# Kernel tuning notes

Hardware: AMD Instinct MI355X
Metric: run time of the kernel (lower is better)

The kernel has to match this reference:

```python
import jax, jax.numpy as jnp
import numpy as np

D_IN = 1024
D_OUT = 1024
N = 4096


def setup_inputs() -> dict:
    key = jax.random.key(0)
    kx, kq, kk, kv = jax.random.split(key, 4)
    x = jax.random.normal(kx, (N, D_IN), dtype=jnp.float32)
    # weights stored as [d_in, d_out] so that x @ W == torch Linear(x)
    s = 1.0 / np.sqrt(D_IN)
    W_q = jax.random.uniform(kq, (D_IN, D_OUT), jnp.float32, -s, s)
    W_k = jax.random.uniform(kk, (D_IN, D_OUT), jnp.float32, -s, s)
    W_v = jax.random.uniform(kv, (D_IN, D_OUT), jnp.float32, -s, s)
    return {"x": x, "W_q": W_q, "W_k": W_k, "W_v": W_v}


def reference(x, W_q, W_k, W_v):
    # x: [N, d_in]; projections -> [N, d_out]
    q = x @ W_q
    k = x @ W_k
    v = x @ W_v
    scale = 1.0 / jnp.sqrt(jnp.asarray(k.shape[-1], dtype=q.dtype))
    scores = (q @ k.T) * scale            # [N, N]
    weights = jax.nn.softmax(scores, axis=-1)
    return weights @ v                     # [N, d_out]
```

## Files before the change

### kernel.cpp

```cpp
#include <hip/hip_runtime.h>
#include <math.h>

typedef _Float16 f16;
typedef __attribute__((ext_vector_type(8))) _Float16 f16x8;
typedef __attribute__((ext_vector_type(4))) _Float16 f16x4;
typedef __attribute__((ext_vector_type(4))) float f32x4;

#define NSEQ 4096
#define DIN 1024
#define DOUT 1024

__device__ __forceinline__ void load16(const void* g, void* l) {
    __builtin_amdgcn_global_load_lds(
        (const __attribute__((address_space(1))) unsigned int*)g,
        (__attribute__((address_space(3))) unsigned int*)l, 16, 0, 0);
}

template <typename OutT, int EPI>
__global__ __launch_bounds__(256, 2)
void gemm_bt(const f16* __restrict__ A, const f16* __restrict__ B,
             OutT* __restrict__ c0, OutT* __restrict__ c1,
             OutT* __restrict__ c2, OutT* __restrict__ c3,
             int M, int N, int K, int lda, int ldb, int ldc, float scale,
             long aStrideZ, long bStrideZ,
             f16* __restrict__ TC, int tz, int ldt, float* __restrict__ Sums)
{
    const int z = blockIdx.z;
    A += (long)z * aStrideZ;
    B += (long)z * bStrideZ;
    OutT* C = z == 0 ? c0 : (z == 1 ? c1 : (z == 2 ? c2 : c3));
    __shared__ f16 As[2 * 128 * 32];
    __shared__ f16 Bs[2 * 128 * 32];

    int gx = gridDim.x;
    int bid = blockIdx.y * gx + blockIdx.x;
    int xcd = bid & 7, s = bid >> 3;
    int px = s & 7, rest = s >> 3;
    int py = rest & 3, chunk = rest >> 2;
    int pg = xcd + (chunk << 3);
    int pcols = gx >> 3;
    int lp = 31 - __clz(pcols);
    int bx = ((pg & (pcols - 1)) << 3) + px;
    int by = ((pg >> lp) << 2) + py;

    const int t    = threadIdx.x;
    const int lane = t & 63;
    const int wave = t >> 6;
    const int wm   = (wave >> 1) * 64;
    const int wn   = (wave & 1) * 64;
    const int tile_m = by * 128;
    const int tile_n = bx * 128;
    const int quad = lane >> 4;
    const int l16  = lane & 15;
    const int srow = t >> 2;
    const int scol = (((t & 3) + srow + (srow >> 2)) & 3) * 8;
    const int qx8 = ((quad - (l16 + (l16 >> 2))) & 3) * 8;

    f32x4 acc[4][4];
#pragma unroll
    for (int i = 0; i < 4; i++)
#pragma unroll
        for (int j = 0; j < 4; j++)
            acc[i][j] = (f32x4){0.f, 0.f, 0.f, 0.f};

    const f16* Ab = A + (long)(tile_m + srow) * lda + scol;
    const f16* Bb = B + (long)(tile_n + srow) * ldb + scol;
    f16* Asd = As + t * 8;
    f16* Bsd = Bs + t * 8;

    for (int k0 = 0; k0 < K; k0 += 64) {
        load16(Ab + k0, Asd);
        load16(Ab + (long)64 * lda + k0, Asd + 2048);
        load16(Ab + k0 + 32, Asd + 4096);
        load16(Ab + (long)64 * lda + k0 + 32, Asd + 4096 + 2048);
        load16(Bb + k0, Bsd);
        load16(Bb + (long)64 * ldb + k0, Bsd + 2048);
        load16(Bb + k0 + 32, Bsd + 4096);
        load16(Bb + (long)64 * ldb + k0 + 32, Bsd + 4096 + 2048);
        __syncthreads();
#pragma unroll
        for (int p = 0; p < 2; p++) {
            f16x8 a[4], b[4];
#pragma unroll
            for (int i = 0; i < 4; i++)
                a[i] = *(const f16x8*)(As + p * 4096 + (wm + i * 16 + l16) * 32 + qx8);
#pragma unroll
            for (int j = 0; j < 4; j++)
                b[j] = *(const f16x8*)(Bs + p * 4096 + (wn + j * 16 + l16) * 32 + qx8);
#pragma unroll
            for (int i = 0; i < 4; i++)
#pragma unroll
                for (int j = 0; j < 4; j++)
                    acc[i][j] = __builtin_amdgcn_mfma_f32_16x16x32_f16(
                        a[i], b[j], acc[i][j], 0, 0, 0);
        }
        __syncthreads();
    }
    if (EPI == 1) {
        if (z == tz) {
#pragma unroll
            for (int i = 0; i < 4; i++)
#pragma unroll
                for (int j = 0; j < 4; j++) {
                    f16x4 o;
#pragma unroll
                    for (int r = 0; r < 4; r++) o[r] = (f16)(acc[i][j][r] * scale);
                    int row0 = tile_m + wm + i * 16 + quad * 4;
                    int col  = tile_n + wn + j * 16 + l16;
                    *(f16x4*)(TC + (long)col * ldt + row0) = o;
                }
        } else {
#pragma unroll
            for (int i = 0; i < 4; i++)
#pragma unroll
                for (int j = 0; j < 4; j++)
#pragma unroll
                    for (int r = 0; r < 4; r++) {
                        int row = tile_m + wm + i * 16 + quad * 4 + r;
                        int col = tile_n + wn + j * 16 + l16;
                        C[(long)row * ldc + col] = (OutT)(acc[i][j][r] * scale);
                    }
        }
    } else if (EPI == 2) {
        const int bxs = bx * 2 + (wn >> 6);
#pragma unroll
        for (int i = 0; i < 4; i++) {
            float rs[4] = {0.f, 0.f, 0.f, 0.f};
#pragma unroll
            for (int j = 0; j < 4; j++)
#pragma unroll
                for (int r = 0; r < 4; r++) {
                    float e = __expf(acc[i][j][r] * scale);
                    int row = tile_m + wm + i * 16 + quad * 4 + r;
                    int col = tile_n + wn + j * 16 + l16;
                    C[(long)row * ldc + col] = (OutT)e;
                    rs[r] += e;
                }
#pragma unroll
            for (int msk = 1; msk < 16; msk <<= 1)
#pragma unroll
                for (int r = 0; r < 4; r++)
                    rs[r] += __shfl_xor(rs[r], msk, 64);
            if (l16 == 0)
#pragma unroll
                for (int r = 0; r < 4; r++) {
                    int row = tile_m + wm + i * 16 + quad * 4 + r;
                    Sums[(long)row * 64 + bxs] = rs[r];
                }
        }
    } else {
#pragma unroll
        for (int i = 0; i < 4; i++)
#pragma unroll
            for (int j = 0; j < 4; j++)
#pragma unroll
                for (int r = 0; r < 4; r++) {
                    int row = tile_m + wm + i * 16 + quad * 4 + r;
                    int col = tile_n + wn + j * 16 + l16;
                    C[(long)row * ldc + col] = (OutT)(acc[i][j][r] * scale);
                }
    }
}

__global__ void prep(const float* __restrict__ x,
                     const float* __restrict__ W0, const float* __restrict__ W1,
                     const float* __restrict__ W2,
                     f16* __restrict__ xb, f16* __restrict__ Wt) {
    if (blockIdx.z == 3) {
        long base = ((long)(blockIdx.y * 16 + blockIdx.x) * 256 + threadIdx.x) * 4;
#pragma unroll
        for (int it = 0; it < 16; it++) {
            long i = base + (long)it * (256 * 256 * 4);
            f32x4 v = *(const f32x4*)(x + i);
            f16x4 o;
            o.x = (f16)v.x; o.y = (f16)v.y; o.z = (f16)v.z; o.w = (f16)v.w;
            *(f16x4*)(xb + i) = o;
        }
        return;
    }
    __shared__ f16 tile[64][65];
    const float* W = blockIdx.z == 0 ? W0 : (blockIdx.z == 1 ? W1 : W2);
    f16* O = Wt + (long)blockIdx.z * DIN * DOUT;
    int r0 = blockIdx.y * 64;
    int c0 = blockIdx.x * 64;
    int tx = threadIdx.x & 63, ty = threadIdx.x >> 6;
#pragma unroll
    for (int i = 0; i < 16; i++)
        tile[ty + i * 4][tx] = (f16)W[(long)(r0 + ty + i * 4) * DOUT + c0 + tx];
    __syncthreads();
#pragma unroll
    for (int i = 0; i < 16; i++)
        O[(long)(c0 + ty + i * 4) * DIN + r0 + tx] = tile[tx][ty + i * 4];
}

__global__ __launch_bounds__(256)
void reduce_norm(const f16* __restrict__ p0, const f16* __restrict__ p1,
                 const f16* __restrict__ p2, const f16* __restrict__ p3,
                 const float* __restrict__ sums, float* __restrict__ out) {
    const int row = blockIdx.x;
    const int lane = threadIdx.x & 63;
    float s = sums[(long)row * 64 + lane];
#pragma unroll
    for (int msk = 1; msk < 64; msk <<= 1) s += __shfl_xor(s, msk, 64);
    const float inv = 1.f / s;
    long i = (long)row * 1024 + threadIdx.x * 4;
    f16x4 a = *(const f16x4*)(p0 + i);
    f16x4 b = *(const f16x4*)(p1 + i);
    f16x4 c = *(const f16x4*)(p2 + i);
    f16x4 d = *(const f16x4*)(p3 + i);
    f32x4 o;
    o.x = (((float)a.x + (float)b.x) + ((float)c.x + (float)d.x)) * inv;
    o.y = (((float)a.y + (float)b.y) + ((float)c.y + (float)d.y)) * inv;
    o.z = (((float)a.z + (float)b.z) + ((float)c.z + (float)d.z)) * inv;
    o.w = (((float)a.w + (float)b.w) + ((float)c.w + (float)d.w)) * inv;
    *(f32x4*)(out + i) = o;
}

extern "C" void kernel_launch(void* const* d_in, const int* in_sizes, int n_in,
                              void* d_out, int out_size, void* d_ws, size_t ws_size,
                              hipStream_t stream) {
    const float* x  = (const float*)d_in[0];
    const float* Wq = (const float*)d_in[1];
    const float* Wk = (const float*)d_in[2];
    const float* Wv = (const float*)d_in[3];
    float* out = (float*)d_out;
    char* ws = (char*)d_ws;
    const size_t MB = 1ull << 20;
    f16* xb  = (f16*)(ws);
    f16* Wt  = (f16*)(ws + 8 * MB);
    f16* Qb  = (f16*)(ws + 14 * MB);
    f16* Kb  = (f16*)(ws + 22 * MB);
    f16* Vt  = (f16*)(ws + 30 * MB);
    f16* S   = (f16*)(ws + 38 * MB);
    f16* scr0 = (f16*)(ws + 70 * MB);
    f16* scr1 = (f16*)(ws + 78 * MB);
    f16* scr2 = (f16*)(ws + 86 * MB);
    f16* scr3 = (f16*)(ws + 94 * MB);
    float* Sums = (float*)(ws);

    prep<<<dim3(16, 16, 4), 256, 0, stream>>>(x, Wq, Wk, Wv, xb, Wt);
    gemm_bt<f16, 1><<<dim3(8, 32, 3), 256, 0, stream>>>(
        xb, Wt, Qb, Kb, Qb, Qb, NSEQ, DOUT, DIN, DIN, DIN, DOUT, 1.0f,
        0, (long)DIN * DOUT, Vt, 2, NSEQ, nullptr);
    gemm_bt<f16, 2><<<dim3(32, 32, 1), 256, 0, stream>>>(
        Qb, Kb, S, S, S, S, NSEQ, NSEQ, DIN, DIN, DIN, NSEQ, 0.03125f,
        0, 0, nullptr, -1, 0, Sums);
    gemm_bt<f16, 0><<<dim3(8, 32, 4), 256, 0, stream>>>(
        S, Vt, scr0, scr1, scr2, scr3, NSEQ, DOUT, 1024, NSEQ, NSEQ, DOUT, 1.0f,
        1024, 1024, nullptr, -1, 0, nullptr);
    reduce_norm<<<4096, 256, 0, stream>>>(scr0, scr1, scr2, scr3, Sums, out);
}
```

Before: 195.9 us.

## Add 256x256-tile 8-wave GEMM with XCD-aware swizzle for score and PV GEMMs

Introduces a new GEMM kernel using 256x256 output tiles, 512 threads, and a split-phase double-buffered LDS pipeline that interleaves global-to-LDS loads with MFMA bursts at raised priority. It also adds a block-index remap that groups tiles per XCD for L2 reuse. The QK^T/exp and the split-K PV GEMMs are switched to it. Larger tiles raise arithmetic intensity and cut redundant operand loads, at the cost of more registers and LDS, fewer blocks, and a more fragile hand-written synchronisation schedule.

Result: slower. 202.7 us (+3.4%).

```diff
diff --git a/kernel.cpp b/kernel.cpp
--- a/kernel.cpp
+++ b/kernel.cpp
@@ -14,6 +14,184 @@
     __builtin_amdgcn_global_load_lds(
         (const __attribute__((address_space(1))) unsigned int*)g,
         (__attribute__((address_space(3))) unsigned int*)l, 16, 0, 0);
+}
+
+#define MEMFENCE asm volatile("" ::: "memory")
+#define BAR() do { MEMFENCE; __builtin_amdgcn_s_barrier(); MEMFENCE; } while (0)
+
+#define MM(I, J, KH, AR) \
+    acc[I][J] = __builtin_amdgcn_mfma_f32_16x16x32_f16(AR[KH], b##J[KH], acc[I][J], 0, 0, 0)
+
+#define MFMA16(I0, I1) \
+    __builtin_amdgcn_s_setprio(1); \
+    MM(I0,0,0,a0); MM(I0,1,0,a0); MM(I0,2,0,a0); MM(I0,3,0,a0); \
+    MM(I1,0,0,a1); MM(I1,1,0,a1); MM(I1,2,0,a1); MM(I1,3,0,a1); \
+    MM(I0,0,1,a0); MM(I0,1,1,a0); MM(I0,2,1,a0); MM(I0,3,1,a0); \
+    MM(I1,0,1,a1); MM(I1,1,1,a1); MM(I1,2,1,a1); MM(I1,3,1,a1); \
+    __builtin_amdgcn_s_setprio(0)
+
+template <typename OutT, int EPI>
+__global__ __launch_bounds__(512, 2)
+void gemm8(const f16* __restrict__ A, const f16* __restrict__ B,
+           OutT* __restrict__ c0, OutT* __restrict__ c1,
+           OutT* __restrict__ c2, OutT* __restrict__ c3,
+           int M, int N, int K, int lda, int ldb, int ldc, float scale,
+           long aStrideZ, long bStrideZ, float* __restrict__ Sums)
+{
+    const int z = blockIdx.z;
+    A += (long)z * aStrideZ;
+    B += (long)z * bStrideZ;
+    OutT* C = z == 0 ? c0 : (z == 1 ? c1 : (z == 2 ? c2 : c3));
+    __shared__ f16 As[2 * 2 * 256 * 32];
+    __shared__ f16 Bs[2 * 2 * 256 * 32];
+
+    const int gx = gridDim.x;
+    const int bid = blockIdx.y * gx + blockIdx.x;
+    int bx, by;
+    if (gx >= 8) {
+        int xcd = bid & 7, s = bid >> 3;
+        int px = s & 7, rest = s >> 3;
+        int py = rest & 3, chunk = rest >> 2;
+        int pg = xcd + (chunk << 3);
+        int pcols = gx >> 3;
+        int lp = 31 - __clz(pcols);
+        bx = ((pg & (pcols - 1)) << 3) + px;
+        by = ((pg >> lp) << 2) + py;
+    } else {
+        int nwg = gx * gridDim.y;
+        int nb = (bid & 7) * (nwg >> 3) + (bid >> 3);
+        bx = nb % gx; by = nb / gx;
+    }
+
+    const int t    = threadIdx.x;
+    const int lane = t & 63;
+    const int w    = t >> 6;
+    const int wm   = (w >> 2) * 128;
+    const int wn   = (w & 3) * 64;
+    const int tile_m = by * 256;
+    const int tile_n = bx * 256;
+    const int quad = lane >> 4;
+    const int l16  = lane & 15;
+    const int srow = t >> 2;
+    const int scol = (((t & 3) + srow + (srow >> 2)) & 3) * 8;
+    const int qx16 = ((quad - (l16 + (l16 >> 2))) & 3) * 16;
+
+    f32x4 acc[8][4];
+#pragma unroll
+    for (int i = 0; i < 8; i++)
+#pragma unroll
+        for (int j = 0; j < 4; j++) acc[i][j] = (f32x4){0.f, 0.f, 0.f, 0.f};
+
+    const f16* Ag = A + (long)(tile_m + srow) * lda + scol;
+    const f16* Bg = B + (long)(tile_n + srow) * ldb + scol;
+    const long a128 = (long)128 * lda, b128 = (long)128 * ldb;
+    char* AsW = (char*)As + t * 16;
+    char* BsW = (char*)Bs + t * 16;
+    const char* aRd = (const char*)As + (wm + l16) * 64 + qx16;
+    const char* bRd = (const char*)Bs + (wn + l16) * 64 + qx16;
+
+    auto stA = [&](int buf, int kh, int rb, int k0) {
+        load16(Ag + k0 + kh * 32 + (long)rb * a128,
+               AsW + buf * 32768 + kh * 16384 + rb * 8192);
+    };
+    auto stB = [&](int buf, int kh, int rb, int k0) {
+        load16(Bg + k0 + kh * 32 + (long)rb * b128,
+               BsW + buf * 32768 + kh * 16384 + rb * 8192);
+    };
+
+    const int nt = K >> 6;
+    stA(0,0,0,0); stA(0,0,1,0); stA(0,1,0,0); stA(0,1,1,0);
+    stB(0,0,0,0); stB(0,0,1,0); stB(0,1,0,0); stB(0,1,1,0);
+    if (nt > 1) {
+        stB(1,0,0,64); stB(1,0,1,64); stB(1,1,0,64); stB(1,1,1,64);
+        asm volatile("s_waitcnt vmcnt(4)" ::: "memory");
+    } else {
+        asm volatile("s_waitcnt vmcnt(0)" ::: "memory");
+    }
+    BAR();
+
+    for (int ti = 0; ti < nt; ++ti) {
+        const int cur = ti & 1;
+        const char* aR = aRd + cur * 32768;
+        const char* bR = bRd + cur * 32768;
+        const int k1 = (ti + 1) << 6;
+        const int k2 = (ti + 2) << 6;
+        f16x8 b0[2], b1[2], b2[2], b3[2], a0[2], a1[2];
+        b0[0] = *(const f16x8*)(bR);          b0[1] = *(const f16x8*)(bR + 16384);
+        b1[0] = *(const f16x8*)(bR + 1024);   b1[1] = *(const f16x8*)(bR + 17408);
+        b2[0] = *(const f16x8*)(bR + 2048);   b2[1] = *(const f16x8*)(bR + 18432);
+        b3[0] = *(const f16x8*)(bR + 3072);   b3[1] = *(const f16x8*)(bR + 19456);
+        a0[0] = *(const f16x8*)(aR);          a0[1] = *(const f16x8*)(aR + 16384);
+        a1[0] = *(const f16x8*)(aR + 1024);   a1[1] = *(const f16x8*)(aR + 17408);
+        if (ti + 1 < nt) { stA(cur ^ 1, 0, 0, k1); stA(cur ^ 1, 0, 1, k1); }
+        BAR();
+        __builtin_amdgcn_sched_barrier(0);
+        MFMA16(0, 1);
+        BAR();
+        a0[0] = *(const f16x8*)(aR + 2048);   a0[1] = *(const f16x8*)(aR + 18432);
+        a1[0] = *(const f16x8*)(aR + 3072);   a1[1] = *(const f16x8*)(aR + 19456);
+        if (ti + 1 < nt) { stA(cur ^ 1, 1, 0, k1); stA(cur ^ 1, 1, 1, k1); }
+        BAR();
+        __builtin_amdgcn_sched_barrier(0);
+        MFMA16(2, 3);
+        BAR();
+        a0[0] = *(const f16x8*)(aR + 4096);   a0[1] = *(const f16x8*)(aR + 20480);
+        a1[0] = *(const f16x8*)(aR + 5120);   a1[1] = *(const f16x8*)(aR + 21504);
+        if (ti + 2 < nt) { stB(cur, 0, 0, k2); stB(cur, 0, 1, k2); }
+        BAR();
+        __builtin_amdgcn_sched_barrier(0);
+        MFMA16(4, 5);
+        BAR();
+        a0[0] = *(const f16x8*)(aR + 6144);   a0[1] = *(const f16x8*)(aR + 22528);
+        a1[0] = *(const f16x8*)(aR + 7168);   a1[1] = *(const f16x8*)(aR + 23552);
+        if (ti + 2 < nt) { stB(cur, 1, 0, k2); stB(cur, 1, 1, k2); }
+        BAR();
+        __builtin_amdgcn_sched_barrier(0);
+        MFMA16(6, 7);
+        if (ti + 2 < nt)      asm volatile("s_waitcnt vmcnt(4)" ::: "memory");
+        else if (ti + 1 < nt) asm volatile("s_waitcnt vmcnt(0)" ::: "memory");
+        BAR();
+    }
+
+    if (EPI == 2) {
+        const int bxs = bx * 4 + (wn >> 6);
+#pragma unroll
+        for (int i = 0; i < 8; i++) {
+            float rs[4] = {0.f, 0.f, 0.f, 0.f};
+#pragma unroll
+            for (int j = 0; j < 4; j++)
+#pragma unroll
+                for (int r = 0; r < 4; r++) {
+                    float e = __expf(acc[i][j][r] * scale);
+                    int row = tile_m + wm + i * 16 + quad * 4 + r;
+                    int col = tile_n + wn + j * 16 + l16;
+                    C[(long)row * ldc + col] = (OutT)e;
+                    rs[r] += e;
+                }
+#pragma unroll
+            for (int msk = 1; msk < 16; msk <<= 1)
+#pragma unroll
+                for (int r = 0; r < 4; r++)
+                    rs[r] += __shfl_xor(rs[r], msk, 64);
+            if (l16 == 0)
+#pragma unroll
+                for (int r = 0; r < 4; r++) {
+                    int row = tile_m + wm + i * 16 + quad * 4 + r;
+                    Sums[(long)row * 64 + bxs] = rs[r];
+                }
+        }
+    } else {
+#pragma unroll
+        for (int i = 0; i < 8; i++)
+#pragma unroll
+            for (int j = 0; j < 4; j++)
+#pragma unroll
+                for (int r = 0; r < 4; r++) {
+                    int row = tile_m + wm + i * 16 + quad * 4 + r;
+                    int col = tile_n + wn + j * 16 + l16;
+                    C[(long)row * ldc + col] = (OutT)(acc[i][j][r] * scale);
+                }
+    }
 }
 
 template <typename OutT, int EPI>
@@ -120,33 +298,6 @@
                         int col = tile_n + wn + j * 16 + l16;
                         C[(long)row * ldc + col] = (OutT)(acc[i][j][r] * scale);
                     }
-        }
-    } else if (EPI == 2) {
-        const int bxs = bx * 2 + (wn >> 6);
-#pragma unroll
-        for (int i = 0; i < 4; i++) {
-            float rs[4] = {0.f, 0.f, 0.f, 0.f};
-#pragma unroll
-            for (int j = 0; j < 4; j++)
-#pragma unroll
-                for (int r = 0; r < 4; r++) {
-                    float e = __expf(acc[i][j][r] * scale);
-                    int row = tile_m + wm + i * 16 + quad * 4 + r;
-                    int col = tile_n + wn + j * 16 + l16;
-                    C[(long)row * ldc + col] = (OutT)e;
-                    rs[r] += e;
-                }
-#pragma unroll
-            for (int msk = 1; msk < 16; msk <<= 1)
-#pragma unroll
-                for (int r = 0; r < 4; r++)
-                    rs[r] += __shfl_xor(rs[r], msk, 64);
-            if (l16 == 0)
-#pragma unroll
-                for (int r = 0; r < 4; r++) {
-                    int row = tile_m + wm + i * 16 + quad * 4 + r;
-                    Sums[(long)row * 64 + bxs] = rs[r];
-                }
         }
     } else {
 #pragma unroll
@@ -242,11 +393,11 @@
     gemm_bt<f16, 1><<<dim3(8, 32, 3), 256, 0, stream>>>(
         xb, Wt, Qb, Kb, Qb, Qb, NSEQ, DOUT, DIN, DIN, DIN, DOUT, 1.0f,
         0, (long)DIN * DOUT, Vt, 2, NSEQ, nullptr);
-    gemm_bt<f16, 2><<<dim3(32, 32, 1), 256, 0, stream>>>(
+    gemm8<f16, 2><<<dim3(16, 16, 1), 512, 0, stream>>>(
         Qb, Kb, S, S, S, S, NSEQ, NSEQ, DIN, DIN, DIN, NSEQ, 0.03125f,
-        0, 0, nullptr, -1, 0, Sums);
-    gemm_bt<f16, 0><<<dim3(8, 32, 4), 256, 0, stream>>>(
+        0, 0, Sums);
+    gemm8<f16, 0><<<dim3(4, 16, 4), 512, 0, stream>>>(
         S, Vt, scr0, scr1, scr2, scr3, NSEQ, DOUT, 1024, NSEQ, NSEQ, DOUT, 1.0f,
-        1024, 1024, nullptr, -1, 0, nullptr);
+        1024, 1024, nullptr);
     reduce_norm<<<4096, 256, 0, stream>>>(scr0, scr1, scr2, scr3, Sums, out);
 }
```

## Double-buffer LDS tiles in GEMM to overlap global loads with MFMA

Applied to the files above, without the earlier changes.

Doubles the shared-memory A/B tile buffers and restructures the K loop into a prologue plus ping-pong scheme. The next K-tile is prefetched with global_load_lds while MFMAs run on the current buffer, hiding global-to-LDS latency behind compute. In exchange, LDS per block doubles to 64KB, which may limit the intended two blocks per CU. Also, the barrier placement must still wait on the async loads, which may serialize part of the overlap.

Result: slower. 214.7 us (+9.6%).

```diff
diff --git a/kernel.cpp b/kernel.cpp
--- a/kernel.cpp
+++ b/kernel.cpp
@@ -29,8 +29,8 @@
     A += (long)z * aStrideZ;
     B += (long)z * bStrideZ;
     OutT* C = z == 0 ? c0 : (z == 1 ? c1 : (z == 2 ? c2 : c3));
-    __shared__ f16 As[2 * 128 * 32];
-    __shared__ f16 Bs[2 * 128 * 32];
+    __shared__ f16 As[2 * 2 * 128 * 32];
+    __shared__ f16 Bs[2 * 2 * 128 * 32];
 
     int gx = gridDim.x;
     int bid = blockIdx.y * gx + blockIdx.x;
@@ -65,28 +65,47 @@
 
     const f16* Ab = A + (long)(tile_m + srow) * lda + scol;
     const f16* Bb = B + (long)(tile_n + srow) * ldb + scol;
+    const long a64 = (long)64 * lda, b64 = (long)64 * ldb;
     f16* Asd = As + t * 8;
     f16* Bsd = Bs + t * 8;
 
-    for (int k0 = 0; k0 < K; k0 += 64) {
-        load16(Ab + k0, Asd);
-        load16(Ab + (long)64 * lda + k0, Asd + 2048);
-        load16(Ab + k0 + 32, Asd + 4096);
-        load16(Ab + (long)64 * lda + k0 + 32, Asd + 4096 + 2048);
-        load16(Bb + k0, Bsd);
-        load16(Bb + (long)64 * ldb + k0, Bsd + 2048);
-        load16(Bb + k0 + 32, Bsd + 4096);
-        load16(Bb + (long)64 * ldb + k0 + 32, Bsd + 4096 + 2048);
-        __syncthreads();
+    const int nt = K >> 6;
+    load16(Ab,            Asd);
+    load16(Ab + a64,      Asd + 2048);
+    load16(Ab + 32,       Asd + 4096);
+    load16(Ab + a64 + 32, Asd + 4096 + 2048);
+    load16(Bb,            Bsd);
+    load16(Bb + b64,      Bsd + 2048);
+    load16(Bb + 32,       Bsd + 4096);
+    load16(Bb + b64 + 32, Bsd + 4096 + 2048);
+    __syncthreads();
+
+    for (int ti = 0; ti < nt; ++ti) {
+        const int cur = ti & 1;
+        if (ti + 1 < nt) {
+            const int k1 = (ti + 1) << 6;
+            f16* Ad = Asd + (cur ^ 1) * 8192;
+            f16* Bd = Bsd + (cur ^ 1) * 8192;
+            load16(Ab + k1,            Ad);
+            load16(Ab + a64 + k1,      Ad + 2048);
+            load16(Ab + k1 + 32,       Ad + 4096);
+            load16(Ab + a64 + k1 + 32, Ad + 4096 + 2048);
+            load16(Bb + k1,            Bd);
+            load16(Bb + b64 + k1,      Bd + 2048);
+            load16(Bb + k1 + 32,       Bd + 4096);
+            load16(Bb + b64 + k1 + 32, Bd + 4096 + 2048);
+        }
+        const f16* Ar = As + cur * 8192;
+        const f16* Br = Bs + cur * 8192;
 #pragma unroll
         for (int p = 0; p < 2; p++) {
             f16x8 a[4], b[4];
 #pragma unroll
             for (int i = 0; i < 4; i++)
-                a[i] = *(const f16x8*)(As + p * 4096 + (wm + i * 16 + l16) * 32 + qx8);
+                a[i] = *(const f16x8*)(Ar + p * 4096 + (wm + i * 16 + l16) * 32 + qx8);
 #pragma unroll
             for (int j = 0; j < 4; j++)
-                b[j] = *(const f16x8*)(Bs + p * 4096 + (wn + j * 16 + l16) * 32 + qx8);
+                b[j] = *(const f16x8*)(Br + p * 4096 + (wn + j * 16 + l16) * 32 + qx8);
 #pragma unroll
             for (int i = 0; i < 4; i++)
 #pragma unroll
```
